# Performance work log

Measured on AMD Instinct MI355X. Metric: run time of the kernel, lower is better.

## Reference

```python
import jax, jax.numpy as jnp
import numpy as np

KR = 2  # nb_row == stride_row
KC = 2  # nb_col == stride_col


def setup_inputs() -> dict:
    key = jax.random.key(0)
    k1, k2, k3 = jax.random.split(key, 3)
    B, C, H, W_ = 32, 32, 128, 128
    F = 64
    OR, OC = H // KR, W_ // KC
    x = jax.random.normal(k1, (B, C, H, W_), dtype=jnp.float32)
    W = jax.random.normal(k2, (F, C, H, W_), dtype=jnp.float32) * 0.05
    b = jax.random.normal(k3, (OR, OC, F), dtype=jnp.float32) * 0.05
    return {"x": x, "W": W, "b": b}


def reference(x, W, b):
    # x: (B, C, H, W), W: (F, C, H, W) -- unshared per-pixel weights
    # per-pixel channel contraction: (B, F, H, W)
    out = jnp.einsum('bchw,fchw->bfhw', x, W)
    B, F, H, Wd = out.shape
    OR, OC = H // KR, Wd // KC
    # stride*avg_pool == exact sum over non-overlapping (KR, KC) patches
    out = out.reshape(B, F, OR, KR, OC, KC).sum(axis=(3, 5))
    # keras does a RAW reshape of b from (OR, OC, F) to (1, F, OR, OC)
    out = out + b.reshape(1, F, OR, OC)
    return jax.nn.relu(out)
```

## Files before the change

kernel.cpp:

```cpp
#include <hip/hip_runtime.h>
#include <stdint.h>


#define CC  32
#define HH  128
#define WWD 128
#define FF  64
#define ORR 64
#define OCC 64
#define CB  4
#define NIT (CC / CB)
#define CSTRIDE (CB * HH * WWD)

#define XBUF 8192

__global__ __launch_bounds__(1024, 4) void lc2d_kernel(
    const float* __restrict__ x, const float* __restrict__ wgt,
    const float* __restrict__ bias, float* __restrict__ out)
{
    __shared__ __align__(16) float Xs[2][XBUF];

    const int tid = threadIdx.x;
    const int id  = blockIdx.x;
    const int oct = ((id & 1) << 1) | (id >> 7);
    const int orr = (id >> 1) & 63;
    const int w0  = oct * 32;
    const int h0  = orr * 2;

    const int lane = tid & 63;
    const int wv   = tid >> 6;
    const int chk  = lane & 7;
    const int sub  = lane >> 3;

    const int r0 = wv * 8 + sub;
    const int r1 = 128 + wv * 8 + sub;
    const float* gx0 = x + (((((r0 & 31) * CC) + (r0 >> 6)) * HH) + h0 + ((r0 >> 5) & 1)) * WWD + w0 + chk * 4;
    const float* gx1 = x + (((((r1 & 31) * CC) + (r1 >> 6)) * HH) + h0 + ((r1 >> 5) & 1)) * WWD + w0 + chk * 4;

    auto issue = [&](int p) {
        __builtin_amdgcn_global_load_lds(
            (const __attribute__((address_space(1))) void*)gx0,
            (__attribute__((address_space(3))) void*)(&Xs[p][wv * 256]), 16, 0, 0);
        __builtin_amdgcn_global_load_lds(
            (const __attribute__((address_space(1))) void*)gx1,
            (__attribute__((address_space(3))) void*)(&Xs[p][4096 + wv * 256]), 16, 0, 0);
        gx0 += CSTRIDE; gx1 += CSTRIDE;
    };

    const int ocg = tid & 7;
    const int bg  = (tid >> 3) & 7;
    const int fg  = wv;
    const int xoff = bg * 128 + ocg * 4;

    const float* wq0 = wgt + ((fg * 4 + 0) * CC * HH + h0) * WWD + w0 + ocg * 4;
    const float* wq1 = wq0 + CC * HH * WWD;
    const float* wq2 = wq1 + CC * HH * WWD;
    const float* wq3 = wq2 + CC * HH * WWD;

    float acc0[4][4], acc1[4][4];
#pragma unroll
    for (int i = 0; i < 4; ++i)
#pragma unroll
        for (int q = 0; q < 4; ++q) { acc0[i][q] = 0.f; acc1[i][q] = 0.f; }

    issue(0);
    __syncthreads();

    for (int it = 0; it < NIT; ++it) {
        const int p = it & 1;
        if (it + 1 < NIT) issue(p ^ 1);

        const float* Xp = Xs[p];
        float4 xa[2][4], wb[2][4];
        {
            const float4* xr = (const float4*)(Xp + xoff);
#pragma unroll
            for (int i = 0; i < 4; ++i) xa[0][i] = xr[i * 8];
            wb[0][0] = *(const float4*)(wq0);
            wb[0][1] = *(const float4*)(wq1);
            wb[0][2] = *(const float4*)(wq2);
            wb[0][3] = *(const float4*)(wq3);
        }
#pragma unroll
        for (int s = 0; s < 2 * CB; ++s) {
            const int cur = s & 1, nxt = cur ^ 1;
            if (s + 1 < 2 * CB) {
                const int sn  = s + 1;
                const int off = ((sn >> 1) * HH + (sn & 1)) * WWD;
                const float4* xr = (const float4*)(Xp + sn * 1024 + xoff);
#pragma unroll
                for (int i = 0; i < 4; ++i) xa[nxt][i] = xr[i * 8];
                wb[nxt][0] = *(const float4*)(wq0 + off);
                wb[nxt][1] = *(const float4*)(wq1 + off);
                wb[nxt][2] = *(const float4*)(wq2 + off);
                wb[nxt][3] = *(const float4*)(wq3 + off);
            }
#pragma unroll
            for (int i = 0; i < 4; ++i)
#pragma unroll
                for (int q = 0; q < 4; ++q) {
                    acc0[i][q] = fmaf(xa[cur][i].x, wb[cur][q].x, acc0[i][q]);
                    acc0[i][q] = fmaf(xa[cur][i].y, wb[cur][q].y, acc0[i][q]);
                    acc1[i][q] = fmaf(xa[cur][i].z, wb[cur][q].z, acc1[i][q]);
                    acc1[i][q] = fmaf(xa[cur][i].w, wb[cur][q].w, acc1[i][q]);
                }
        }
        wq0 += CSTRIDE; wq1 += CSTRIDE; wq2 += CSTRIDE; wq3 += CSTRIDE;
        __syncthreads();
    }

    const int oc0 = oct * 16 + ocg * 2;
#pragma unroll
    for (int q = 0; q < 4; ++q) {
        const int f = fg * 4 + q;
        const float2 bv = *(const float2*)(bias + f * (ORR * OCC) + orr * OCC + oc0);
#pragma unroll
        for (int i = 0; i < 4; ++i) {
            const int b = bg * 4 + i;
            float2 o;
            o.x = fmaxf(acc0[i][q] + bv.x, 0.f);
            o.y = fmaxf(acc1[i][q] + bv.y, 0.f);
            *(float2*)(out + (((b * FF + f) * ORR + orr) * OCC) + oc0) = o;
        }
    }
}

extern "C" void kernel_launch(void* const* d_in, const int* in_sizes, int n_in,
                              void* d_out, int out_size, void* d_ws, size_t ws_size,
                              hipStream_t stream) {
    (void)in_sizes; (void)n_in; (void)d_ws; (void)ws_size; (void)out_size;
    const float* x    = (const float*)d_in[0];
    const float* wgt  = (const float*)d_in[1];
    const float* bias = (const float*)d_in[2];
    float* out        = (float*)d_out;
    lc2d_kernel<<<dim3(256, 1, 1), dim3(1024, 1, 1), 0, stream>>>(x, wgt, bias, out);
}
```

Before: 269.6 us.

## Split filters across two blocks, doubling grid and halving block size

Each block now covers 32 of the 64 filters, so the grid grows from 256 to 512 blocks of 512 threads, and each thread issues four global-to-LDS loads instead of two to fill the same x tile. This spreads the work over more of the GPU's compute units and gives more blocks per unit for latency hiding. The cost is that every x tile is now fetched twice, once per filter half. Empty asm memory barriers are also added to pin the order of loads and FMAs within the loop.

```diff
diff --git a/kernel.cpp b/kernel.cpp
--- a/kernel.cpp
+++ b/kernel.cpp
@@ -11,19 +11,22 @@
 #define CB  4
 #define NIT (CC / CB)
 #define CSTRIDE (CB * HH * WWD)
+#define CHW (CC * HH * WWD)
 
 #define XBUF 8192
 
-__global__ __launch_bounds__(1024, 4) void lc2d_kernel(
+__global__ __launch_bounds__(512, 4) void lc2d_kernel(
     const float* __restrict__ x, const float* __restrict__ wgt,
     const float* __restrict__ bias, float* __restrict__ out)
 {
     __shared__ __align__(16) float Xs[2][XBUF];
 
-    const int tid = threadIdx.x;
-    const int id  = blockIdx.x;
-    const int oct = ((id & 1) << 1) | (id >> 7);
-    const int orr = (id >> 1) & 63;
+    const int tid  = threadIdx.x;
+    const int id   = blockIdx.x;
+    const int fblk = id >> 8;
+    const int low  = id & 255;
+    const int oct = ((low & 1) << 1) | (low >> 7);
+    const int orr = (low >> 1) & 63;
     const int w0  = oct * 32;
     const int h0  = orr * 2;
 
@@ -32,30 +35,31 @@
     const int chk  = lane & 7;
     const int sub  = lane >> 3;
 
-    const int r0 = wv * 8 + sub;
-    const int r1 = 128 + wv * 8 + sub;
-    const float* gx0 = x + (((((r0 & 31) * CC) + (r0 >> 6)) * HH) + h0 + ((r0 >> 5) & 1)) * WWD + w0 + chk * 4;
-    const float* gx1 = x + (((((r1 & 31) * CC) + (r1 >> 6)) * HH) + h0 + ((r1 >> 5) & 1)) * WWD + w0 + chk * 4;
+    const float* gx[4];
+#pragma unroll
+    for (int j = 0; j < 4; ++j) {
+        const int r = j * 64 + wv * 8 + sub;
+        gx[j] = x + (((((r & 31) * CC) + (r >> 6)) * HH) + h0 + ((r >> 5) & 1)) * WWD + w0 + chk * 4;
+    }
 
     auto issue = [&](int p) {
-        __builtin_amdgcn_global_load_lds(
-            (const __attribute__((address_space(1))) void*)gx0,
-            (__attribute__((address_space(3))) void*)(&Xs[p][wv * 256]), 16, 0, 0);
-        __builtin_amdgcn_global_load_lds(
-            (const __attribute__((address_space(1))) void*)gx1,
-            (__attribute__((address_space(3))) void*)(&Xs[p][4096 + wv * 256]), 16, 0, 0);
-        gx0 += CSTRIDE; gx1 += CSTRIDE;
+#pragma unroll
+        for (int j = 0; j < 4; ++j) {
+            __builtin_amdgcn_global_load_lds(
+                (const __attribute__((address_space(1))) void*)gx[j],
+                (__attribute__((address_space(3))) void*)(&Xs[p][j * 2048 + wv * 256]), 16, 0, 0);
+            gx[j] += CSTRIDE;
+        }
     };
 
     const int ocg = tid & 7;
     const int bg  = (tid >> 3) & 7;
-    const int fg  = wv;
     const int xoff = bg * 128 + ocg * 4;
 
-    const float* wq0 = wgt + ((fg * 4 + 0) * CC * HH + h0) * WWD + w0 + ocg * 4;
-    const float* wq1 = wq0 + CC * HH * WWD;
-    const float* wq2 = wq1 + CC * HH * WWD;
-    const float* wq3 = wq2 + CC * HH * WWD;
+    const float* wq[4];
+#pragma unroll
+    for (int q = 0; q < 4; ++q)
+        wq[q] = wgt + (size_t)(fblk * 32 + wv * 4 + q) * CHW + (h0 * WWD) + w0 + ocg * 4;
 
     float acc0[4][4], acc1[4][4];
 #pragma unroll
@@ -76,11 +80,10 @@
             const float4* xr = (const float4*)(Xp + xoff);
 #pragma unroll
             for (int i = 0; i < 4; ++i) xa[0][i] = xr[i * 8];
-            wb[0][0] = *(const float4*)(wq0);
-            wb[0][1] = *(const float4*)(wq1);
-            wb[0][2] = *(const float4*)(wq2);
-            wb[0][3] = *(const float4*)(wq3);
+#pragma unroll
+            for (int q = 0; q < 4; ++q) wb[0][q] = *(const float4*)(wq[q]);
         }
+        asm volatile("" ::: "memory");
 #pragma unroll
         for (int s = 0; s < 2 * CB; ++s) {
             const int cur = s & 1, nxt = cur ^ 1;
@@ -90,11 +93,10 @@
                 const float4* xr = (const float4*)(Xp + sn * 1024 + xoff);
 #pragma unroll
                 for (int i = 0; i < 4; ++i) xa[nxt][i] = xr[i * 8];
-                wb[nxt][0] = *(const float4*)(wq0 + off);
-                wb[nxt][1] = *(const float4*)(wq1 + off);
-                wb[nxt][2] = *(const float4*)(wq2 + off);
-                wb[nxt][3] = *(const float4*)(wq3 + off);
+#pragma unroll
+                for (int q = 0; q < 4; ++q) wb[nxt][q] = *(const float4*)(wq[q] + off);
             }
+            asm volatile("" ::: "memory");
 #pragma unroll
             for (int i = 0; i < 4; ++i)
 #pragma unroll
@@ -105,14 +107,15 @@
                     acc1[i][q] = fmaf(xa[cur][i].w, wb[cur][q].w, acc1[i][q]);
                 }
         }
-        wq0 += CSTRIDE; wq1 += CSTRIDE; wq2 += CSTRIDE; wq3 += CSTRIDE;
+#pragma unroll
+        for (int q = 0; q < 4; ++q) wq[q] += CSTRIDE;
         __syncthreads();
     }
 
     const int oc0 = oct * 16 + ocg * 2;
 #pragma unroll
     for (int q = 0; q < 4; ++q) {
-        const int f = fg * 4 + q;
+        const int f = fblk * 32 + wv * 4 + q;
         const float2 bv = *(const float2*)(bias + f * (ORR * OCC) + orr * OCC + oc0);
 #pragma unroll
         for (int i = 0; i < 4; ++i) {
@@ -133,5 +136,5 @@
     const float* wgt  = (const float*)d_in[1];
     const float* bias = (const float*)d_in[2];
     float* out        = (float*)d_out;
-    lc2d_kernel<<<dim3(256, 1, 1), dim3(1024, 1, 1), 0, stream>>>(x, wgt, bias, out);
+    lc2d_kernel<<<dim3(512, 1, 1), dim3(512, 1, 1), 0, stream>>>(x, wgt, bias, out);
 }
```

New measurement: 670.3 us. 149% more time.
